# Performance work log

Measured on AMD Instinct MI355X. Metric: run time of the kernel, lower is better.

## Reference

```python
import jax, jax.numpy as jnp
import numpy as np

N = 100000      # nodes
E = 1600000     # edges (avg degree 16)
K = 3           # num_stacks
T = 4           # num_layers
H = 16          # hidden channels (conv1 out)
C = 1           # num_classes
BN_EPS = 1e-5


def setup_inputs() -> dict:
    key = jax.random.key(0)
    ks = jax.random.split(key, 14)
    s = 0.1
    return {
        "x": jax.random.normal(ks[0], (N, 1), jnp.float32),
        "edge_index": jax.random.randint(ks[1], (2, E), 0, N, dtype=jnp.int64),
        "edge_weight": jax.random.uniform(ks[2], (E,), jnp.float32),
        # conv1 (ARMAConv 1->16, K stacks, shared weights)
        "w1_init": jax.random.normal(ks[3], (K, 1, H), jnp.float32) * s,
        "w1_w":    jax.random.normal(ks[4], (K, H, H), jnp.float32) * s,
        "w1_root": jax.random.normal(ks[5], (K, 1, H), jnp.float32) * s,
        "w1_b":    jax.random.normal(ks[6], (K, H), jnp.float32) * s,
        "bn1_g": jnp.ones((H,), jnp.float32),
        "bn1_b": jnp.zeros((H,), jnp.float32),
        # conv2 (ARMAConv 16->1, act=None)
        "w2_init": jax.random.normal(ks[7], (K, H, C), jnp.float32) * s,
        "w2_w":    jax.random.normal(ks[8], (K, C, C), jnp.float32) * s,
        "w2_root": jax.random.normal(ks[9], (K, H, C), jnp.float32) * s,
        "w2_b":    jax.random.normal(ks[10], (K, C), jnp.float32) * s,
        # end linear 1->1
        "lin_w": jax.random.normal(ks[11], (C, C), jnp.float32) * s,
        "lin_b": jnp.zeros((C,), jnp.float32),
    }


def _arma_conv(x, src, dst, norm, init_w, w, root_w, bias, act):
    """PyG ARMAConv with shared weights. x: [N,Fin] -> [N,Fout]."""
    n = x.shape[0]
    # root/skip term (dropout is identity in eval); bias broadcast per stack
    root = jnp.einsum('ni,kio->nko', x, root_w) + bias[None, :, :]  # [N,K,Fout]
    out = jnp.einsum('ni,kio->nko', x, init_w)                      # t=0 transform
    for t in range(T):
        if t > 0:
            out = jnp.einsum('nki,kio->nko', out, w)                # shared weight
        msg = out[src] * norm[:, None, None]                        # [E,K,Fout]
        out = jax.ops.segment_sum(msg, dst, num_segments=n)         # A_hat @ out
        out = out + root
        if act:
            out = jax.nn.relu(out)
    return out.mean(axis=1)  # average over stacks


def reference(x, edge_index, edge_weight, w1_init, w1_w, w1_root, w1_b,
              bn1_g, bn1_b, w2_init, w2_w, w2_root, w2_b, lin_w, lin_b):
    src, dst = edge_index[0], edge_index[1]
    n = x.shape[0]
    # gcn_norm without self loops
    deg = jax.ops.segment_sum(edge_weight, dst, num_segments=n)
    dis = jnp.where(deg > 0, 1.0 / jnp.sqrt(deg), 0.0)
    norm = dis[src] * edge_weight * dis[dst]

    h = _arma_conv(x, src, dst, norm, w1_init, w1_w, w1_root, w1_b, act=True)
    # BatchNorm1d over node dim (batch statistics, deterministic)
    mu = h.mean(axis=0)
    var = h.var(axis=0)
    h = (h - mu) / jnp.sqrt(var + BN_EPS) * bn1_g + bn1_b
    h = jax.nn.relu(h)
    # dropout is identity in eval
    h = _arma_conv(h, src, dst, norm, w2_init, w2_w, w2_root, w2_b, act=False)
    h = h @ lin_w.T + lin_b
    return jax.nn.sigmoid(h)
```

## Files before the change

### kernel.cpp

```cpp
#include <hip/hip_runtime.h>
#include <hip/hip_bf16.h>
#include <math.h>

#define CAP 48


__global__ void zero_kernel(float* p, int n) {
    int i = blockIdx.x * blockDim.x + threadIdx.x;
    if (i < n) p[i] = 0.f;
}

__global__ void bucket_insert_part(const int* __restrict__ ei, const float* __restrict__ ew,
                                   int* __restrict__ len, int2* __restrict__ pcsr,
                                   int E, int n) {
    int part = blockIdx.x & 7;
    int chunk = blockIdx.x >> 3;
    int base = chunk * 2048;
    int pw = (n + 7) >> 3;
    int lo = part * pw;
    int hi = lo + pw; hi = hi < n ? hi : n;
    int end = base + 2048; end = end < E ? end : E;
    for (int i = base + threadIdx.x; i < end; i += 256) {
        int d = ei[E + i];
        if (d >= lo && d < hi) {
            int s = ei[i];
            float w = ew[i];
            int pos = atomicAdd(&len[d], 1);
            if (pos < CAP) pcsr[d * CAP + pos] = make_int2(s, __float_as_int(w));
        }
    }
}

__global__ void wdeg_dis_w(const int2* __restrict__ pcsr, const int* __restrict__ len,
                           float* __restrict__ dis, int n) {
    int wid = (int)((blockIdx.x * blockDim.x + threadIdx.x) >> 6);
    int lane = threadIdx.x & 63;
    if (wid >= n) return;
    int L = len[wid]; L = L < CAP ? L : CAP;
    float w = (lane < L) ? __int_as_float(pcsr[wid * CAP + lane].y) : 0.f;
#pragma unroll
    for (int off = 32; off >= 1; off >>= 1) w += __shfl_xor(w, off, 64);
    if (lane == 0) dis[wid] = (w > 0.f) ? (1.0f / sqrtf(w)) : 0.f;
}

__global__ void normk_w(int2* __restrict__ pcsr, const int* __restrict__ len,
                        const float* __restrict__ dis, int n) {
    int wid = (int)((blockIdx.x * blockDim.x + threadIdx.x) >> 6);
    int lane = threadIdx.x & 63;
    if (wid >= n) return;
    int L = len[wid]; L = L < CAP ? L : CAP;
    float dn = dis[wid];
    if (lane < L) {
        int idx = wid * CAP + lane;
        int2 e = pcsr[idx];
        pcsr[idx].y = __float_as_int(__int_as_float(e.y) * dn * dis[e.x]);
    }
}


__global__ void aggx(const float* __restrict__ x, const int* __restrict__ len,
                     const int2* __restrict__ pcsr, float* __restrict__ y, int n) {
    int node = blockIdx.x * blockDim.x + threadIdx.x;
    if (node >= n) return;
    const long long* csr8 = (const long long*)pcsr;
    int p = node * CAP;
    int L = len[node]; L = L < CAP ? L : CAP;
    int end = p + L;
    float a0 = 0.f, a1 = 0.f;
    for (; p + 15 < end; p += 16) {
        long long e[16];
#pragma unroll
        for (int j = 0; j < 16; j++) e[j] = csr8[p + j];
        float q[16];
#pragma unroll
        for (int j = 0; j < 16; j++) q[j] = x[(int)e[j]];
#pragma unroll
        for (int j = 0; j < 8; j++) {
            a0 += q[2 * j] * __int_as_float((int)(e[2 * j] >> 32));
            a1 += q[2 * j + 1] * __int_as_float((int)(e[2 * j + 1] >> 32));
        }
    }
    for (; p + 7 < end; p += 8) {
        long long e[8];
#pragma unroll
        for (int j = 0; j < 8; j++) e[j] = csr8[p + j];
#pragma unroll
        for (int j = 0; j < 8; j++) {
            float q = x[(int)e[j]];
            (j & 1 ? a1 : a0) += q * __int_as_float((int)(e[j] >> 32));
        }
    }
    for (; p < end; p++) {
        long long e = csr8[p];
        a0 += x[(int)e] * __int_as_float((int)(e >> 32));
    }
    y[node] = a0 + a1;
}

__global__ void init48(const float* __restrict__ x, const float* __restrict__ y,
                       const float* __restrict__ w_init, const float* __restrict__ w_root,
                       const float* __restrict__ w_b, __hip_bfloat16* __restrict__ P, int n) {
    unsigned t = blockIdx.x * blockDim.x + threadIdx.x;
    if (t >= (unsigned)n * 64u) return;
    unsigned node = t >> 6, c = t & 63;
    if (c >= 48) return;
    float v = fmaxf(y[node] * w_init[c] + x[node] * w_root[c] + w_b[c], 0.f);
    P[node * 64u + c] = __float2bfloat16(v);
}

__global__ void __launch_bounds__(256) agg48u(
    const __hip_bfloat16* __restrict__ P, const float* __restrict__ W,
    const float* __restrict__ x, const float* __restrict__ w_root,
    const float* __restrict__ w_b, const int* __restrict__ len,
    const int2* __restrict__ pcsr, __hip_bfloat16* __restrict__ Pout, int n) {
    int wid = (int)((blockIdx.x * blockDim.x + threadIdx.x) >> 6);
    int lane = threadIdx.x & 63;
    if (wid >= n || lane >= 48) return;
    int k = lane >> 4, o = lane & 15;
    float wv[16];
#pragma unroll
    for (int i = 0; i < 16; i++) wv[i] = W[k * 256 + i * 16 + o];

    const long long* csr8 = (const long long*)pcsr;
    int p = wid * CAP;
    int L = len[wid]; L = L < CAP ? L : CAP;
    int end = p + L;
    float a0 = 0.f, a1 = 0.f, a2 = 0.f, a3 = 0.f;
    for (; p + 15 < end; p += 16) {
        long long e[16];
#pragma unroll
        for (int j = 0; j < 16; j++) e[j] = csr8[p + j];
        float q[16];
#pragma unroll
        for (int j = 0; j < 16; j++)
            q[j] = __bfloat162float(P[(unsigned)(int)e[j] * 64u + lane]);
#pragma unroll
        for (int j = 0; j < 4; j++) {
            a0 += q[4 * j]     * __int_as_float((int)(e[4 * j]     >> 32));
            a1 += q[4 * j + 1] * __int_as_float((int)(e[4 * j + 1] >> 32));
            a2 += q[4 * j + 2] * __int_as_float((int)(e[4 * j + 2] >> 32));
            a3 += q[4 * j + 3] * __int_as_float((int)(e[4 * j + 3] >> 32));
        }
    }
    for (; p + 7 < end; p += 8) {
        long long e[8];
#pragma unroll
        for (int j = 0; j < 8; j++) e[j] = csr8[p + j];
        float q[8];
#pragma unroll
        for (int j = 0; j < 8; j++)
            q[j] = __bfloat162float(P[(unsigned)(int)e[j] * 64u + lane]);
#pragma unroll
        for (int j = 0; j < 2; j++) {
            a0 += q[4 * j]     * __int_as_float((int)(e[4 * j]     >> 32));
            a1 += q[4 * j + 1] * __int_as_float((int)(e[4 * j + 1] >> 32));
            a2 += q[4 * j + 2] * __int_as_float((int)(e[4 * j + 2] >> 32));
            a3 += q[4 * j + 3] * __int_as_float((int)(e[4 * j + 3] >> 32));
        }
    }
    for (; p + 3 < end; p += 4) {
        long long e[4];
#pragma unroll
        for (int j = 0; j < 4; j++) e[j] = csr8[p + j];
#pragma unroll
        for (int j = 0; j < 4; j++) {
            float q = __bfloat162float(P[(unsigned)(int)e[j] * 64u + lane]);
            (j == 0 ? a0 : j == 1 ? a1 : j == 2 ? a2 : a3) += q * __int_as_float((int)(e[j] >> 32));
        }
    }
    for (; p < end; p++) {
        long long e = csr8[p];
        a0 += __bfloat162float(P[(unsigned)(int)e * 64u + lane]) * __int_as_float((int)(e >> 32));
    }
    float S = (a0 + a1) + (a2 + a3);

    float acc = 0.f;
    int base = lane & 48;
#pragma unroll
    for (int i = 0; i < 16; i++) {
        float sv = __shfl(S, base + i, 64);
        acc += sv * wv[i];
    }
    float v = acc + x[wid] * w_root[lane] + w_b[lane];
    Pout[(unsigned)wid * 64u + lane] = __float2bfloat16(fmaxf(v, 0.f));
}


__global__ void bn_stats(const __hip_bfloat16* __restrict__ P, float* __restrict__ acc, int n) {
    int tid = threadIdx.x;
    int c = tid & 15;
    int rowSlot = (int)((blockIdx.x * blockDim.x + tid) >> 4);
    int rowStride = (int)((gridDim.x * blockDim.x) >> 4);
    float s1 = 0.f, s2 = 0.f;
    for (int r = rowSlot; r < n; r += rowStride) {
        const __hip_bfloat16* row = &P[(unsigned)r * 64u];
        float h = (__bfloat162float(row[c]) + __bfloat162float(row[16 + c]) +
                   __bfloat162float(row[32 + c])) * (1.f / 3.f);
        s1 += h;
        s2 += h * h;
    }
    __shared__ float sh[256];
    sh[tid] = s1; __syncthreads();
    for (int off = 128; off >= 16; off >>= 1) { if (tid < off) sh[tid] += sh[tid + off]; __syncthreads(); }
    if (tid < 16) atomicAdd(&acc[tid], sh[tid]);
    __syncthreads();
    sh[tid] = s2; __syncthreads();
    for (int off = 128; off >= 16; off >>= 1) { if (tid < off) sh[tid] += sh[tid + off]; __syncthreads(); }
    if (tid < 16) atomicAdd(&acc[16 + tid], sh[tid]);
}

__global__ void bn_cvec(const float* __restrict__ acc, const float* __restrict__ g,
                        const float* __restrict__ b, int n,
                        const float* __restrict__ w2w, const float* __restrict__ w2i,
                        const float* __restrict__ w2r, const float* __restrict__ w2b,
                        float* __restrict__ coef, float* __restrict__ cvec) {
    int c = threadIdx.x;
    const float inv3 = 1.f / 3.f;
    if (c < 16) {
        float mu = acc[c] / (float)n;
        float var = acc[16 + c] / (float)n - mu * mu;
        float sc = g[c] / sqrtf(var + 1e-5f);
        coef[c] = sc;
        coef[16 + c] = b[c] - mu * sc;
        float wk0 = w2w[0], wk1 = w2w[1], wk2 = w2w[2];
        float wks[3] = {wk0, wk1, wk2};
        float psi = 0.f, r3 = 0.f, r2 = 0.f, r1 = 0.f, r0 = 0.f;
#pragma unroll
        for (int k = 0; k < 3; k++) {
            float w = wks[k], w2_ = w * w, w3 = w2_ * w;
            psi += w3 * w2i[k * 16 + c];
            float rr = w2r[k * 16 + c];
            r3 += w3 * rr; r2 += w2_ * rr; r1 += w * rr; r0 += rr;
        }
        cvec[c] = psi * inv3;
        cvec[16 + c] = r3 * inv3;
        cvec[32 + c] = r2 * inv3;
        cvec[48 + c] = r1 * inv3;
        cvec[64 + c] = r0 * inv3;
    } else if (c == 16) {
        float wk0 = w2w[0], wk1 = w2w[1], wk2 = w2w[2];
        float wks[3] = {wk0, wk1, wk2};
        float b3 = 0.f, b2 = 0.f, b1 = 0.f, b0 = 0.f;
#pragma unroll
        for (int k = 0; k < 3; k++) {
            float w = wks[k], w2_ = w * w, w3 = w2_ * w;
            float bb = w2b[k];
            b3 += w3 * bb; b2 += w2_ * bb; b1 += w * bb; b0 += bb;
        }
        cvec[80] = b3 * inv3; cvec[81] = b2 * inv3; cvec[82] = b1 * inv3; cvec[83] = b0 * inv3;
    }
}


__global__ void conv2_init(const __hip_bfloat16* __restrict__ P, const float* __restrict__ coef,
                           const float* __restrict__ cvec,
                           float* __restrict__ z, float4* __restrict__ R, int n) {
    unsigned node = blockIdx.x * blockDim.x + threadIdx.x;
    if (node >= (unsigned)n) return;
    const __hip_bfloat16* row = &P[node * 64u];
    float zz = 0.f, r3 = cvec[80], r2 = cvec[81], r1 = cvec[82], r0 = cvec[83];
#pragma unroll
    for (int c = 0; c < 16; c++) {
        float h = (__bfloat162float(row[c]) + __bfloat162float(row[16 + c]) +
                   __bfloat162float(row[32 + c])) * (1.f / 3.f);
        float hb = fmaxf(h * coef[c] + coef[16 + c], 0.f);
        zz += hb * cvec[c];
        r3 += hb * cvec[16 + c];
        r2 += hb * cvec[32 + c];
        r1 += hb * cvec[48 + c];
        r0 += hb * cvec[64 + c];
    }
    z[node] = zz;
    R[node] = make_float4(r3, r2, r1, r0);
}

template<int FINAL>
__global__ void horner(const float* __restrict__ zin, const float* __restrict__ R, int comp,
                       const int* __restrict__ len, const int2* __restrict__ pcsr,
                       float* __restrict__ zout, const float* __restrict__ lw,
                       const float* __restrict__ lb, int n) {
    int node = blockIdx.x * blockDim.x + threadIdx.x;
    if (node >= n) return;
    const long long* csr8 = (const long long*)pcsr;
    int p = node * CAP;
    int L = len[node]; L = L < CAP ? L : CAP;
    int end = p + L;
    float a0 = 0.f, a1 = 0.f;
    for (; p + 15 < end; p += 16) {
        long long e[16];
#pragma unroll
        for (int j = 0; j < 16; j++) e[j] = csr8[p + j];
        float q[16];
#pragma unroll
        for (int j = 0; j < 16; j++) q[j] = zin[(int)e[j]];
#pragma unroll
        for (int j = 0; j < 8; j++) {
            a0 += q[2 * j] * __int_as_float((int)(e[2 * j] >> 32));
            a1 += q[2 * j + 1] * __int_as_float((int)(e[2 * j + 1] >> 32));
        }
    }
    for (; p + 7 < end; p += 8) {
        long long e[8];
#pragma unroll
        for (int j = 0; j < 8; j++) e[j] = csr8[p + j];
#pragma unroll
        for (int j = 0; j < 8; j++) {
            float q = zin[(int)e[j]];
            (j & 1 ? a1 : a0) += q * __int_as_float((int)(e[j] >> 32));
        }
    }
    for (; p < end; p++) {
        long long e = csr8[p];
        a0 += zin[(int)e] * __int_as_float((int)(e >> 32));
    }
    float v = (a0 + a1) + R[(unsigned)node * 4u + comp];
    if (FINAL) {
        float t = v * lw[0] + lb[0];
        zout[node] = 1.f / (1.f + expf(-t));
    } else {
        zout[node] = v;
    }
}


extern "C" void kernel_launch(void* const* d_in, const int* in_sizes, int n_in,
                              void* d_out, int out_size, void* d_ws, size_t ws_size,
                              hipStream_t stream) {
    const float* x = (const float*)d_in[0];
    const int* ei = (const int*)d_in[1];
    const float* ew = (const float*)d_in[2];
    const float* w1_init = (const float*)d_in[3];
    const float* w1_w = (const float*)d_in[4];
    const float* w1_root = (const float*)d_in[5];
    const float* w1_b = (const float*)d_in[6];
    const float* bn1_g = (const float*)d_in[7];
    const float* bn1_b = (const float*)d_in[8];
    const float* w2_init = (const float*)d_in[9];
    const float* w2_w = (const float*)d_in[10];
    const float* w2_root = (const float*)d_in[11];
    const float* w2_b = (const float*)d_in[12];
    const float* lin_w = (const float*)d_in[13];
    const float* lin_b = (const float*)d_in[14];

    const int N = in_sizes[0];
    const int E = in_sizes[2];
    float* out = (float*)d_out;

    char* ws = (char*)d_ws;
    size_t off = 0;
    auto alloc = [&](size_t bytes) {
        void* p = ws + off;
        off += (bytes + 15) & ~(size_t)15;
        return p;
    };
    int*   len     = (int*)  alloc((size_t)N * 4);
    float* bn_acc  = (float*)alloc(32 * 4);
    float* bn_coef = (float*)alloc(32 * 4);
    float* cvec    = (float*)alloc(96 * 4);
    float* dis     = (float*)alloc((size_t)N * 4);
    float* y1      = (float*)alloc((size_t)N * 4);
    float* zA      = (float*)alloc((size_t)N * 4);
    float* zB      = (float*)alloc((size_t)N * 4);
    float4* Rbuf   = (float4*)alloc((size_t)N * 16);
    int2*  pcsr    = (int2*) alloc((size_t)N * CAP * 8);
    __hip_bfloat16* bufP = (__hip_bfloat16*)alloc((size_t)N * 64 * 2);
    __hip_bfloat16* bufQ = (__hip_bfloat16*)alloc((size_t)N * 64 * 2);
    (void)ws_size;

    const int BS = 256;
    int gN = (N + BS - 1) / BS;
    int gW = (N + 3) / 4;

    zero_kernel<<<(N + 32 + BS - 1) / BS, BS, 0, stream>>>((float*)len, N + 32);

    int nChunks = (E + 2047) / 2048;
    bucket_insert_part<<<8 * nChunks, BS, 0, stream>>>(ei, ew, len, pcsr, E, N);
    wdeg_dis_w<<<gW, BS, 0, stream>>>(pcsr, len, dis, N);
    normk_w<<<gW, BS, 0, stream>>>(pcsr, len, dis, N);

    aggx<<<gN, BS, 0, stream>>>(x, len, pcsr, y1, N);
    int g64 = (N * 64 + BS - 1) / BS;
    init48<<<g64, BS, 0, stream>>>(x, y1, w1_init, w1_root, w1_b, bufP, N);
    agg48u<<<gW, BS, 0, stream>>>(bufP, w1_w, x, w1_root, w1_b, len, pcsr, bufQ, N);
    agg48u<<<gW, BS, 0, stream>>>(bufQ, w1_w, x, w1_root, w1_b, len, pcsr, bufP, N);
    agg48u<<<gW, BS, 0, stream>>>(bufP, w1_w, x, w1_root, w1_b, len, pcsr, bufQ, N);

    bn_stats<<<512, 256, 0, stream>>>(bufQ, bn_acc, N);
    bn_cvec<<<1, 64, 0, stream>>>(bn_acc, bn1_g, bn1_b, N, w2_w, w2_init, w2_root, w2_b,
                                  bn_coef, cvec);

    conv2_init<<<gN, BS, 0, stream>>>(bufQ, bn_coef, cvec, zA, Rbuf, N);
    horner<0><<<gN, BS, 0, stream>>>(zA, (const float*)Rbuf, 0, len, pcsr, zB, lin_w, lin_b, N);
    horner<0><<<gN, BS, 0, stream>>>(zB, (const float*)Rbuf, 1, len, pcsr, zA, lin_w, lin_b, N);
    horner<0><<<gN, BS, 0, stream>>>(zA, (const float*)Rbuf, 2, len, pcsr, zB, lin_w, lin_b, N);
    horner<1><<<gN, BS, 0, stream>>>(zB, (const float*)Rbuf, 3, len, pcsr, out, lin_w, lin_b, N);
}
```

Baseline: 404.3 us.

## Fuse edge normalization with x aggregation and use fixed padded gathers

Merges the normalization kernel and the x-aggregation kernel into one wave-per-node pass that writes normalized weights and reduces w*x through shuffles. Degree scale and x are packed into one float2 array so each edge needs a single gather. The padded CSR is zeroed first so the 48-channel aggregation can always run 16 or 32 edges without remainder loops, with padding edges having weight 0 and source 0. This adds a large memset over the whole padded CSR each call and wasted gathers for low-degree nodes.

```diff
diff --git a/kernel.cpp b/kernel.cpp
--- a/kernel.cpp
+++ b/kernel.cpp
@@ -32,7 +32,7 @@
 }
 
 __global__ void wdeg_dis_w(const int2* __restrict__ pcsr, const int* __restrict__ len,
-                           float* __restrict__ dis, int n) {
+                           const float* __restrict__ x, float2* __restrict__ dx, int n) {
     int wid = (int)((blockIdx.x * blockDim.x + threadIdx.x) >> 6);
     int lane = threadIdx.x & 63;
     if (wid >= n) return;
@@ -40,62 +40,33 @@
     float w = (lane < L) ? __int_as_float(pcsr[wid * CAP + lane].y) : 0.f;
 #pragma unroll
     for (int off = 32; off >= 1; off >>= 1) w += __shfl_xor(w, off, 64);
-    if (lane == 0) dis[wid] = (w > 0.f) ? (1.0f / sqrtf(w)) : 0.f;
-}
-
-__global__ void normk_w(int2* __restrict__ pcsr, const int* __restrict__ len,
-                        const float* __restrict__ dis, int n) {
+    if (lane == 0) {
+        float d = (w > 0.f) ? (1.0f / sqrtf(w)) : 0.f;
+        dx[wid] = make_float2(d, x[wid]);
+    }
+}
+
+__global__ void normagg(int2* __restrict__ pcsr, const int* __restrict__ len,
+                        const float2* __restrict__ dx, float* __restrict__ y, int n) {
     int wid = (int)((blockIdx.x * blockDim.x + threadIdx.x) >> 6);
     int lane = threadIdx.x & 63;
     if (wid >= n) return;
     int L = len[wid]; L = L < CAP ? L : CAP;
-    float dn = dis[wid];
+    float dn = dx[wid].x;
+    float part = 0.f;
     if (lane < L) {
         int idx = wid * CAP + lane;
         int2 e = pcsr[idx];
-        pcsr[idx].y = __float_as_int(__int_as_float(e.y) * dn * dis[e.x]);
-    }
-}
-
-
-__global__ void aggx(const float* __restrict__ x, const int* __restrict__ len,
-                     const int2* __restrict__ pcsr, float* __restrict__ y, int n) {
-    int node = blockIdx.x * blockDim.x + threadIdx.x;
-    if (node >= n) return;
-    const long long* csr8 = (const long long*)pcsr;
-    int p = node * CAP;
-    int L = len[node]; L = L < CAP ? L : CAP;
-    int end = p + L;
-    float a0 = 0.f, a1 = 0.f;
-    for (; p + 15 < end; p += 16) {
-        long long e[16];
-#pragma unroll
-        for (int j = 0; j < 16; j++) e[j] = csr8[p + j];
-        float q[16];
-#pragma unroll
-        for (int j = 0; j < 16; j++) q[j] = x[(int)e[j]];
-#pragma unroll
-        for (int j = 0; j < 8; j++) {
-            a0 += q[2 * j] * __int_as_float((int)(e[2 * j] >> 32));
-            a1 += q[2 * j + 1] * __int_as_float((int)(e[2 * j + 1] >> 32));
-        }
-    }
-    for (; p + 7 < end; p += 8) {
-        long long e[8];
-#pragma unroll
-        for (int j = 0; j < 8; j++) e[j] = csr8[p + j];
-#pragma unroll
-        for (int j = 0; j < 8; j++) {
-            float q = x[(int)e[j]];
-            (j & 1 ? a1 : a0) += q * __int_as_float((int)(e[j] >> 32));
-        }
-    }
-    for (; p < end; p++) {
-        long long e = csr8[p];
-        a0 += x[(int)e] * __int_as_float((int)(e >> 32));
-    }
-    y[node] = a0 + a1;
-}
+        float2 sdx = dx[e.x];
+        float wn = __int_as_float(e.y) * dn * sdx.x;
+        pcsr[idx].y = __float_as_int(wn);
+        part = wn * sdx.y;
+    }
+#pragma unroll
+    for (int off = 32; off >= 1; off >>= 1) part += __shfl_xor(part, off, 64);
+    if (lane == 0) y[wid] = part;
+}
+
 
 __global__ void init48(const float* __restrict__ x, const float* __restrict__ y,
                        const float* __restrict__ w_init, const float* __restrict__ w_root,
@@ -108,7 +79,7 @@
     P[node * 64u + c] = __float2bfloat16(v);
 }
 
-__global__ void __launch_bounds__(256) agg48u(
+__global__ void __launch_bounds__(256, 4) agg48v(
     const __hip_bfloat16* __restrict__ P, const float* __restrict__ W,
     const float* __restrict__ x, const float* __restrict__ w_root,
     const float* __restrict__ w_b, const int* __restrict__ len,
@@ -122,14 +93,13 @@
     for (int i = 0; i < 16; i++) wv[i] = W[k * 256 + i * 16 + o];
 
     const long long* csr8 = (const long long*)pcsr;
-    int p = wid * CAP;
+    int base = wid * CAP;
     int L = len[wid]; L = L < CAP ? L : CAP;
-    int end = p + L;
     float a0 = 0.f, a1 = 0.f, a2 = 0.f, a3 = 0.f;
-    for (; p + 15 < end; p += 16) {
+    {
         long long e[16];
 #pragma unroll
-        for (int j = 0; j < 16; j++) e[j] = csr8[p + j];
+        for (int j = 0; j < 16; j++) e[j] = csr8[base + j];
         float q[16];
 #pragma unroll
         for (int j = 0; j < 16; j++)
@@ -142,43 +112,33 @@
             a3 += q[4 * j + 3] * __int_as_float((int)(e[4 * j + 3] >> 32));
         }
     }
-    for (; p + 7 < end; p += 8) {
-        long long e[8];
-#pragma unroll
-        for (int j = 0; j < 8; j++) e[j] = csr8[p + j];
-        float q[8];
-#pragma unroll
-        for (int j = 0; j < 8; j++)
+    if (L > 16) {
+        long long e[16];
+#pragma unroll
+        for (int j = 0; j < 16; j++) e[j] = csr8[base + 16 + j];
+        float q[16];
+#pragma unroll
+        for (int j = 0; j < 16; j++)
             q[j] = __bfloat162float(P[(unsigned)(int)e[j] * 64u + lane]);
 #pragma unroll
-        for (int j = 0; j < 2; j++) {
+        for (int j = 0; j < 4; j++) {
             a0 += q[4 * j]     * __int_as_float((int)(e[4 * j]     >> 32));
             a1 += q[4 * j + 1] * __int_as_float((int)(e[4 * j + 1] >> 32));
             a2 += q[4 * j + 2] * __int_as_float((int)(e[4 * j + 2] >> 32));
             a3 += q[4 * j + 3] * __int_as_float((int)(e[4 * j + 3] >> 32));
         }
     }
-    for (; p + 3 < end; p += 4) {
-        long long e[4];
-#pragma unroll
-        for (int j = 0; j < 4; j++) e[j] = csr8[p + j];
-#pragma unroll
-        for (int j = 0; j < 4; j++) {
-            float q = __bfloat162float(P[(unsigned)(int)e[j] * 64u + lane]);
-            (j == 0 ? a0 : j == 1 ? a1 : j == 2 ? a2 : a3) += q * __int_as_float((int)(e[j] >> 32));
-        }
-    }
-    for (; p < end; p++) {
+    for (int p = base + 32; p < base + L; p++) {
         long long e = csr8[p];
         a0 += __bfloat162float(P[(unsigned)(int)e * 64u + lane]) * __int_as_float((int)(e >> 32));
     }
     float S = (a0 + a1) + (a2 + a3);
 
     float acc = 0.f;
-    int base = lane & 48;
+    int bl = lane & 48;
 #pragma unroll
     for (int i = 0; i < 16; i++) {
-        float sv = __shfl(S, base + i, 64);
+        float sv = __shfl(S, bl + i, 64);
         acc += sv * wv[i];
     }
     float v = acc + x[wid] * w_root[lane] + w_b[lane];
@@ -357,7 +317,7 @@
     float* bn_acc  = (float*)alloc(32 * 4);
     float* bn_coef = (float*)alloc(32 * 4);
     float* cvec    = (float*)alloc(96 * 4);
-    float* dis     = (float*)alloc((size_t)N * 4);
+    float2* dx     = (float2*)alloc((size_t)N * 8);
     float* y1      = (float*)alloc((size_t)N * 4);
     float* zA      = (float*)alloc((size_t)N * 4);
     float* zB      = (float*)alloc((size_t)N * 4);
@@ -371,19 +331,19 @@
     int gN = (N + BS - 1) / BS;
     int gW = (N + 3) / 4;
 
+    hipMemsetAsync(pcsr, 0, (size_t)N * CAP * 8, stream);
     zero_kernel<<<(N + 32 + BS - 1) / BS, BS, 0, stream>>>((float*)len, N + 32);
 
     int nChunks = (E + 2047) / 2048;
     bucket_insert_part<<<8 * nChunks, BS, 0, stream>>>(ei, ew, len, pcsr, E, N);
-    wdeg_dis_w<<<gW, BS, 0, stream>>>(pcsr, len, dis, N);
-    normk_w<<<gW, BS, 0, stream>>>(pcsr, len, dis, N);
-
-    aggx<<<gN, BS, 0, stream>>>(x, len, pcsr, y1, N);
+    wdeg_dis_w<<<gW, BS, 0, stream>>>(pcsr, len, x, dx, N);
+    normagg<<<gW, BS, 0, stream>>>(pcsr, len, dx, y1, N);
+
     int g64 = (N * 64 + BS - 1) / BS;
     init48<<<g64, BS, 0, stream>>>(x, y1, w1_init, w1_root, w1_b, bufP, N);
-    agg48u<<<gW, BS, 0, stream>>>(bufP, w1_w, x, w1_root, w1_b, len, pcsr, bufQ, N);
-    agg48u<<<gW, BS, 0, stream>>>(bufQ, w1_w, x, w1_root, w1_b, len, pcsr, bufP, N);
-    agg48u<<<gW, BS, 0, stream>>>(bufP, w1_w, x, w1_root, w1_b, len, pcsr, bufQ, N);
+    agg48v<<<gW, BS, 0, stream>>>(bufP, w1_w, x, w1_root, w1_b, len, pcsr, bufQ, N);
+    agg48v<<<gW, BS, 0, stream>>>(bufQ, w1_w, x, w1_root, w1_b, len, pcsr, bufP, N);
+    agg48v<<<gW, BS, 0, stream>>>(bufP, w1_w, x, w1_root, w1_b, len, pcsr, bufQ, N);
 
     bn_stats<<<512, 256, 0, stream>>>(bufQ, bn_acc, N);
     bn_cvec<<<1, 64, 0, stream>>>(bn_acc, bn1_g, bn1_b, N, w2_w, w2_init, w2_root, w2_b,
```

Result: no change. 408.6 us (+1.1%).
